# Performance work log

Measured on AMD Instinct MI355X. Metric: run time of the kernel, lower is better.

Reference implementation:

```python
import jax, jax.numpy as jnp
import numpy as np

N, D, F = 10000, 16, 256  # nodes, uniform degree, feature dim (F_in == F_out required by module)


def setup_inputs() -> dict:
    key = jax.random.key(0)
    ks = jax.random.split(key, 8)
    s = 0.05  # small param scale (xavier-like) to keep exp() in a sane range
    return {
        "nodes": jax.random.normal(ks[0], (N, F), jnp.float32),
        "neighbors": jax.random.normal(ks[1], (N, D, F), jnp.float32),
        "aspects": jax.random.normal(ks[2], (N, D, F), jnp.float32),
        "Wp": jax.random.normal(ks[3], (F, F), jnp.float32) * s,      # linear_proj.weight
        "Wa": jax.random.normal(ks[4], (F, 2 * F), jnp.float32) * s,  # aspect_linear_proj.weight
        "ba": jnp.zeros((F,), jnp.float32),                           # aspect_linear_proj.bias
        "a_src": jax.random.normal(ks[5], (F,), jnp.float32) * s,     # scoring_fn_source
        "a_tgt": jax.random.normal(ks[6], (F,), jnp.float32) * s,     # scoring_fn_target
        "bias": jnp.zeros((F,), jnp.float32),                         # output bias
    }


def reference(nodes, neighbors, aspects, Wp, Wa, ba, a_src, a_tgt, bias):
    # target scores from projected node features: [N]
    nodes_proj = nodes @ Wp.T                                   # [N, F]
    scores_target = (nodes_proj * a_tgt).sum(-1)                # [N]

    # project neighbors and aspects with the shared linear_proj: [N, D, F]
    n_proj = jnp.einsum('ndf,gf->ndg', neighbors, Wp)
    a_proj = jnp.einsum('ndf,gf->ndg', aspects, Wp)

    # linear aspects method: concat projected features, then aspect Linear
    na = jnp.concatenate([n_proj, a_proj], axis=-1)             # [N, D, 2F]
    na_proj = jnp.einsum('ndk,fk->ndf', na, Wa) + ba            # [N, D, F]

    scores_source = (na_proj * a_src).sum(-1)                   # [N, D]
    scores = jax.nn.leaky_relu(scores_source + scores_target[:, None], 0.2)

    # module uses raw exp / (sum + 1e-16), not max-subtracted softmax
    e = jnp.exp(scores)                                         # [N, D]
    attn = e / (e.sum(axis=1, keepdims=True) + 1e-16)

    out = jnp.einsum('ndf,nd->nf', n_proj, attn)                # [N, F]
    return jax.nn.elu(out + bias)
```

## Files before the change

kernel.cpp:

```cpp
#include <hip/hip_runtime.h>
#include <hip/hip_bf16.h>
#include <math.h>

#define NN 10000
#define DD 16
#define FF 256

typedef float f32x4 __attribute__((ext_vector_type(4)));
#define DOT4(a, b) ((a)[0]*(b)[0] + (a)[1]*(b)[1] + (a)[2]*(b)[2] + (a)[3]*(b)[3])


__global__ __launch_bounds__(256) void k_pre1(
    const float* __restrict__ Wp, const float* __restrict__ Wa,
    const float* __restrict__ a_src, const float* __restrict__ a_tgt,
    float* __restrict__ part) {
  const int t = threadIdx.x, b = blockIdx.x;
  float s1 = 0.f, s2 = 0.f, vt = 0.f;
  #pragma unroll
  for (int k = 0; k < 16; ++k) {
    const int f = b * 16 + k;
    const float as = a_src[f];
    s1 += as * Wa[f * 2 * FF + t];
    s2 += as * Wa[f * 2 * FF + FF + t];
    vt += a_tgt[f] * Wp[f * FF + t];
  }
  part[(b * 3 + 0) * FF + t] = s1;
  part[(b * 3 + 1) * FF + t] = s2;
  part[(b * 3 + 2) * FF + t] = vt;
}

__global__ __launch_bounds__(256) void k_pre2(
    const float* __restrict__ Wp, const float* __restrict__ ba,
    const float* __restrict__ a_src, const float* __restrict__ part,
    float* __restrict__ pre) {
  __shared__ float w1[FF], w2[FF];
  __shared__ float pu1[8][32], pu2[8][32];
  const int t = threadIdx.x;

  float a0 = 0.f, a1 = 0.f, a2 = 0.f;
  #pragma unroll
  for (int b = 0; b < 16; ++b) {
    a0 += part[(b * 3 + 0) * FF + t];
    a1 += part[(b * 3 + 1) * FF + t];
    a2 += part[(b * 3 + 2) * FF + t];
  }
  w1[t] = a0; w2[t] = a1;
  if (blockIdx.x == 0) {
    pre[t] = a2;
    if (t < 64) {
      float cp = 0.f;
      #pragma unroll
      for (int k = 0; k < 4; ++k) cp += ba[t + 64 * k] * a_src[t + 64 * k];
      #pragma unroll
      for (int o = 32; o > 0; o >>= 1) cp += __shfl_xor(cp, o);
      if (t == 0) pre[3 * FF] = cp;
    }
  }
  __syncthreads();

  const int tc = t & 31;
  const int gc = t >> 5;
  const int tt = blockIdx.x * 32 + tc;
  float u1 = 0.f, u2 = 0.f;
  #pragma unroll 4
  for (int g = gc * 32; g < gc * 32 + 32; ++g) {
    const float wpg = Wp[g * FF + tt];
    u1 += w1[g] * wpg;
    u2 += w2[g] * wpg;
  }
  pu1[gc][tc] = u1; pu2[gc][tc] = u2;
  __syncthreads();
  if (t < 32) {
    float r1 = 0.f, r2 = 0.f;
    #pragma unroll
    for (int k = 0; k < 8; ++k) { r1 += pu1[k][t]; r2 += pu2[k][t]; }
    pre[FF + blockIdx.x * 32 + t] = r1;
    pre[2 * FF + blockIdx.x * 32 + t] = r2;
  }
}

__global__ __launch_bounds__(256) void k_attn_agg(
    const float* __restrict__ nodes, const float* __restrict__ neighbors,
    const float* __restrict__ aspects, const float* __restrict__ pre,
    float* __restrict__ agg) {
  const int n = blockIdx.x;
  const int tid = threadIdx.x;
  const int wid = tid >> 6;
  const int lane = tid & 63;

  __shared__ float nb[DD][FF];
  __shared__ float sc[DD];

  const f32x4* nbg = (const f32x4*)(neighbors + (size_t)n * DD * FF);
  const f32x4* asg = (const f32x4*)(aspects + (size_t)n * DD * FF);
  const f32x4* ndp = (const f32x4*)(nodes + (size_t)n * FF);

  f32x4 nbv[4], asv[4];
  #pragma unroll
  for (int k = 0; k < 4; ++k)
    nbv[k] = __builtin_nontemporal_load(&nbg[(wid + 4 * k) * (FF / 4) + lane]);
  #pragma unroll
  for (int k = 0; k < 4; ++k)
    asv[k] = __builtin_nontemporal_load(&asg[(wid + 4 * k) * (FF / 4) + lane]);
  f32x4 nv = ndp[lane];

  const f32x4 u1v = ((const f32x4*)(pre + FF))[lane];
  const f32x4 u2v = ((const f32x4*)(pre + 2 * FF))[lane];
  const f32x4 vtv = ((const f32x4*)(pre))[lane];
  const float c0 = pre[3 * FF];

  #pragma unroll
  for (int k = 0; k < 4; ++k)
    ((f32x4*)&nb[wid + 4 * k][0])[lane] = nbv[k];

  float p[4];
  #pragma unroll
  for (int k = 0; k < 4; ++k)
    p[k] = DOT4(nbv[k], u1v) + DOT4(asv[k], u2v);
  float st = DOT4(nv, vtv);

  #pragma unroll
  for (int o = 32; o > 0; o >>= 1) {
    p[0] += __shfl_xor(p[0], o);
    p[1] += __shfl_xor(p[1], o);
    p[2] += __shfl_xor(p[2], o);
    p[3] += __shfl_xor(p[3], o);
    st   += __shfl_xor(st, o);
  }
  if (lane == 0) {
    #pragma unroll
    for (int k = 0; k < 4; ++k) sc[wid + 4 * k] = p[k] + st + c0;
  }
  __syncthreads();

  float e[DD];
  float esum = 0.f;
  #pragma unroll
  for (int d = 0; d < DD; ++d) {
    float s = sc[d];
    s = s > 0.f ? s : 0.2f * s;
    float ev = __expf(s);
    e[d] = ev;
    esum += ev;
  }
  const float inv = 1.f / (esum + 1e-16f);

  float acc = 0.f;
  #pragma unroll
  for (int d = 0; d < DD; ++d) acc += e[d] * nb[d][tid];
  agg[(size_t)n * FF + tid] = acc * inv;
}

#define TN 16
__global__ __launch_bounds__(256) void k_proj_out(
    const float* __restrict__ Wp, const float* __restrict__ bias,
    float* __restrict__ out) {
  const int t = threadIdx.x;
  const int n0 = blockIdx.x * TN;
  __shared__ float ag[TN][FF];

  #pragma unroll
  for (int i = 0; i < TN; ++i)
    ag[i][t] = out[(size_t)(n0 + i) * FF + t];
  __syncthreads();

  float acc[TN];
  #pragma unroll
  for (int i = 0; i < TN; ++i) acc[i] = 0.f;

  const float4* wrow = (const float4*)(Wp + (size_t)t * FF);
  for (int f4 = 0; f4 < FF / 4; ++f4) {
    float4 w = wrow[f4];
    #pragma unroll
    for (int i = 0; i < TN; ++i) {
      float4 a = ((const float4*)&ag[i][0])[f4];
      acc[i] += a.x * w.x + a.y * w.y + a.z * w.z + a.w * w.w;
    }
  }

  const float b = bias[t];
  #pragma unroll
  for (int i = 0; i < TN; ++i) {
    float v = acc[i] + b;
    out[(size_t)(n0 + i) * FF + t] = v > 0.f ? v : expm1f(v);
  }
}

extern "C" void kernel_launch(void* const* d_in, const int* in_sizes, int n_in,
                              void* d_out, int out_size, void* d_ws, size_t ws_size,
                              hipStream_t stream) {
  const float* nodes     = (const float*)d_in[0];
  const float* neighbors = (const float*)d_in[1];
  const float* aspects   = (const float*)d_in[2];
  const float* Wp        = (const float*)d_in[3];
  const float* Wa        = (const float*)d_in[4];
  const float* ba        = (const float*)d_in[5];
  const float* a_src     = (const float*)d_in[6];
  const float* a_tgt     = (const float*)d_in[7];
  const float* bias      = (const float*)d_in[8];
  float* out = (float*)d_out;
  float* pre = (float*)d_ws;

  float* part = out + (size_t)NN * FF - 16 * 3 * FF;

  k_pre1<<<16, 256, 0, stream>>>(Wp, Wa, a_src, a_tgt, part);
  k_pre2<<<8, 256, 0, stream>>>(Wp, ba, a_src, part, pre);
  k_attn_agg<<<NN, 256, 0, stream>>>(nodes, neighbors, aspects, pre, out);
  k_proj_out<<<NN / TN, 256, 0, stream>>>(Wp, bias, out);
}
```

Before: 116.0 us.

## Fuse attention aggregation with output projection into one per-tile kernel

Merges the per-node attention/aggregation kernel and the output projection kernel into one kernel. Each block now loops over 16 nodes, keeping their aggregated features in shared memory, then applies the Wp projection, bias and ELU. This removes the global round trip of the intermediate aggregate and one kernel launch. The cost is a much smaller grid and a serial per-node loop with barriers, which cuts memory-level parallelism for the dominant neighbor and aspect stream.

```diff
diff --git a/kernel.cpp b/kernel.cpp
--- a/kernel.cpp
+++ b/kernel.cpp
@@ -5,6 +5,7 @@
 #define NN 10000
 #define DD 16
 #define FF 256
+#define TN 16
 
 typedef float f32x4 __attribute__((ext_vector_type(4)));
 #define DOT4(a, b) ((a)[0]*(b)[0] + (a)[1]*(b)[1] + (a)[2]*(b)[2] + (a)[3]*(b)[3])
@@ -79,110 +80,101 @@
   }
 }
 
-__global__ __launch_bounds__(256) void k_attn_agg(
+__global__ __launch_bounds__(256) void k_fused(
     const float* __restrict__ nodes, const float* __restrict__ neighbors,
     const float* __restrict__ aspects, const float* __restrict__ pre,
-    float* __restrict__ agg) {
-  const int n = blockIdx.x;
+    const float* __restrict__ Wp, const float* __restrict__ bias,
+    float* __restrict__ out) {
   const int tid = threadIdx.x;
   const int wid = tid >> 6;
   const int lane = tid & 63;
+  const int n0 = blockIdx.x * TN;
 
   __shared__ float nb[DD][FF];
+  __shared__ float ag[TN][FF];
   __shared__ float sc[DD];
-
-  const f32x4* nbg = (const f32x4*)(neighbors + (size_t)n * DD * FF);
-  const f32x4* asg = (const f32x4*)(aspects + (size_t)n * DD * FF);
-  const f32x4* ndp = (const f32x4*)(nodes + (size_t)n * FF);
-
-  f32x4 nbv[4], asv[4];
-  #pragma unroll
-  for (int k = 0; k < 4; ++k)
-    nbv[k] = __builtin_nontemporal_load(&nbg[(wid + 4 * k) * (FF / 4) + lane]);
-  #pragma unroll
-  for (int k = 0; k < 4; ++k)
-    asv[k] = __builtin_nontemporal_load(&asg[(wid + 4 * k) * (FF / 4) + lane]);
-  f32x4 nv = ndp[lane];
 
   const f32x4 u1v = ((const f32x4*)(pre + FF))[lane];
   const f32x4 u2v = ((const f32x4*)(pre + 2 * FF))[lane];
   const f32x4 vtv = ((const f32x4*)(pre))[lane];
   const float c0 = pre[3 * FF];
 
-  #pragma unroll
-  for (int k = 0; k < 4; ++k)
-    ((f32x4*)&nb[wid + 4 * k][0])[lane] = nbv[k];
-
-  float p[4];
-  #pragma unroll
-  for (int k = 0; k < 4; ++k)
-    p[k] = DOT4(nbv[k], u1v) + DOT4(asv[k], u2v);
-  float st = DOT4(nv, vtv);
-
-  #pragma unroll
-  for (int o = 32; o > 0; o >>= 1) {
-    p[0] += __shfl_xor(p[0], o);
-    p[1] += __shfl_xor(p[1], o);
-    p[2] += __shfl_xor(p[2], o);
-    p[3] += __shfl_xor(p[3], o);
-    st   += __shfl_xor(st, o);
-  }
-  if (lane == 0) {
-    #pragma unroll
-    for (int k = 0; k < 4; ++k) sc[wid + 4 * k] = p[k] + st + c0;
-  }
-  __syncthreads();
-
-  float e[DD];
-  float esum = 0.f;
-  #pragma unroll
-  for (int d = 0; d < DD; ++d) {
-    float s = sc[d];
-    s = s > 0.f ? s : 0.2f * s;
-    float ev = __expf(s);
-    e[d] = ev;
-    esum += ev;
-  }
-  const float inv = 1.f / (esum + 1e-16f);
-
-  float acc = 0.f;
-  #pragma unroll
-  for (int d = 0; d < DD; ++d) acc += e[d] * nb[d][tid];
-  agg[(size_t)n * FF + tid] = acc * inv;
-}
-
-#define TN 16
-__global__ __launch_bounds__(256) void k_proj_out(
-    const float* __restrict__ Wp, const float* __restrict__ bias,
-    float* __restrict__ out) {
-  const int t = threadIdx.x;
-  const int n0 = blockIdx.x * TN;
-  __shared__ float ag[TN][FF];
-
-  #pragma unroll
-  for (int i = 0; i < TN; ++i)
-    ag[i][t] = out[(size_t)(n0 + i) * FF + t];
-  __syncthreads();
+  for (int i = 0; i < TN; ++i) {
+    const int n = n0 + i;
+    const f32x4* nbg = (const f32x4*)(neighbors + (size_t)n * DD * FF);
+    const f32x4* asg = (const f32x4*)(aspects + (size_t)n * DD * FF);
+
+    f32x4 nbv[4], asv[4];
+    #pragma unroll
+    for (int k = 0; k < 4; ++k)
+      nbv[k] = __builtin_nontemporal_load(&nbg[(wid + 4 * k) * (FF / 4) + lane]);
+    #pragma unroll
+    for (int k = 0; k < 4; ++k)
+      asv[k] = __builtin_nontemporal_load(&asg[(wid + 4 * k) * (FF / 4) + lane]);
+    const f32x4 nv = ((const f32x4*)(nodes + (size_t)n * FF))[lane];
+
+    #pragma unroll
+    for (int k = 0; k < 4; ++k)
+      ((f32x4*)&nb[wid + 4 * k][0])[lane] = nbv[k];
+
+    float p[4];
+    #pragma unroll
+    for (int k = 0; k < 4; ++k)
+      p[k] = DOT4(nbv[k], u1v) + DOT4(asv[k], u2v);
+    float st = DOT4(nv, vtv);
+
+    #pragma unroll
+    for (int o = 32; o > 0; o >>= 1) {
+      p[0] += __shfl_xor(p[0], o);
+      p[1] += __shfl_xor(p[1], o);
+      p[2] += __shfl_xor(p[2], o);
+      p[3] += __shfl_xor(p[3], o);
+      st   += __shfl_xor(st, o);
+    }
+    if (lane == 0) {
+      #pragma unroll
+      for (int k = 0; k < 4; ++k) sc[wid + 4 * k] = p[k] + st + c0;
+    }
+    __syncthreads();
+
+    float e[DD];
+    float esum = 0.f;
+    #pragma unroll
+    for (int d = 0; d < DD; ++d) {
+      float s = sc[d];
+      s = s > 0.f ? s : 0.2f * s;
+      float ev = __expf(s);
+      e[d] = ev;
+      esum += ev;
+    }
+    const float inv = 1.f / (esum + 1e-16f);
+
+    float acc = 0.f;
+    #pragma unroll
+    for (int d = 0; d < DD; ++d) acc += e[d] * nb[d][tid];
+    ag[i][tid] = acc * inv;
+    __syncthreads();
+  }
 
   float acc[TN];
   #pragma unroll
   for (int i = 0; i < TN; ++i) acc[i] = 0.f;
 
-  const float4* wrow = (const float4*)(Wp + (size_t)t * FF);
+  const f32x4* wrow = (const f32x4*)(Wp + (size_t)tid * FF);
   for (int f4 = 0; f4 < FF / 4; ++f4) {
-    float4 w = wrow[f4];
+    const f32x4 w = wrow[f4];
     #pragma unroll
     for (int i = 0; i < TN; ++i) {
-      float4 a = ((const float4*)&ag[i][0])[f4];
-      acc[i] += a.x * w.x + a.y * w.y + a.z * w.z + a.w * w.w;
-    }
-  }
-
-  const float b = bias[t];
+      const f32x4 a = ((const f32x4*)&ag[i][0])[f4];
+      acc[i] += DOT4(a, w);
+    }
+  }
+
+  const float b = bias[tid];
   #pragma unroll
   for (int i = 0; i < TN; ++i) {
     float v = acc[i] + b;
-    out[(size_t)(n0 + i) * FF + t] = v > 0.f ? v : expm1f(v);
+    out[(size_t)(n0 + i) * FF + tid] = v > 0.f ? v : expm1f(v);
   }
 }
 
@@ -205,6 +197,5 @@
 
   k_pre1<<<16, 256, 0, stream>>>(Wp, Wa, a_src, a_tgt, part);
   k_pre2<<<8, 256, 0, stream>>>(Wp, ba, a_src, part, pre);
-  k_attn_agg<<<NN, 256, 0, stream>>>(nodes, neighbors, aspects, pre, out);
-  k_proj_out<<<NN / TN, 256, 0, stream>>>(Wp, bias, out);
-}
+  k_fused<<<NN / TN, 256, 0, stream>>>(nodes, neighbors, aspects, pre, Wp, bias, out);
+}
```

After: 112.8 us. -2.8%, faster.
